# Kernel tuning notes

Measured on AMD Instinct MI355X. Metric: run time of the kernel, lower is better.

## Reference

```python
import jax, jax.numpy as jnp
import numpy as np

HEADS = 16
DIM_HEAD = 128
DIM = HEADS * DIM_HEAD          # hidden_size = 2048
SEGMENT_LEN = 496
NUM_LONGTERM = 16
NUM_PERSIST = 16
C = SEGMENT_LEN + NUM_LONGTERM  # total_segment_len = 512 (window width)
EPS = 1e-6
THETA = 10000.0
NEG = -jnp.finfo(jnp.float32).max


def _rope(t, cos, sin):
    # t: [b, h, n, d]; cos/sin: [n, d]; interleaved (rotate-half on adjacent pairs)
    t2 = t.reshape(t.shape[:-1] + (DIM_HEAD // 2, 2))
    rot = jnp.stack((-t2[..., 1], t2[..., 0]), axis=-1).reshape(t.shape)
    return t * cos + rot * sin


def _attn_bias():
    # queries: [m_len longterm-mem tokens | segment tokens]
    # keys:    [p_len persistent | m_len longterm-mem | segment tokens]
    q_len = C
    k_len = C + NUM_PERSIST
    pq = NUM_LONGTERM
    pk = NUM_PERSIST + NUM_LONGTERM
    bias = jnp.full((q_len, k_len), NEG, dtype=jnp.float32)
    bias = bias.at[:, :pk].set(0.0)  # everyone attends to the prefix
    sq = q_len - pq
    causal = jnp.tril(jnp.ones((sq, sq), dtype=bool))
    bias = bias.at[pq:, pk:].set(jnp.where(causal, 0.0, NEG))
    return bias


def setup_inputs() -> dict:
    key = jax.random.key(0)
    k1, k2, k3, k4 = jax.random.split(key, 4)
    b, n = 2, 4096  # n must be a multiple of C=512
    return {
        "x": jax.random.normal(k1, (b, n, DIM), dtype=jnp.float32),
        "norm_w": jnp.ones((DIM,), dtype=jnp.float32),
        "w_qkv": jax.random.normal(k2, (3 * DIM, DIM), dtype=jnp.float32) * 0.02,
        "w_out": jax.random.normal(k3, (DIM, DIM), dtype=jnp.float32) * 0.02,
        "pm": jax.random.normal(k4, (2, HEADS, NUM_PERSIST, DIM_HEAD), dtype=jnp.float32) * 0.02,
    }


def reference(x, norm_w, w_qkv, w_out, pm):
    b, n, d = x.shape
    # RMSNorm
    xn = x * jax.lax.rsqrt(jnp.mean(x * x, axis=-1, keepdims=True) + EPS) * norm_w
    # qkv projection (Linear, no bias)
    qkv = xn @ w_qkv.T
    q, k, v = jnp.split(qkv, 3, axis=-1)

    def to_heads(t):  # [b, n, h*d] -> [b, h, n, d]
        return t.reshape(b, n, HEADS, DIM_HEAD).transpose(0, 2, 1, 3)

    q, k, v = to_heads(q), to_heads(k), to_heads(v)

    # RoPE over full sequence positions 0..n-1 (before windowing)
    inv_freq = 1.0 / (THETA ** (jnp.arange(0, DIM_HEAD, 2, dtype=jnp.float32) / DIM_HEAD))
    freqs = jnp.arange(n, dtype=jnp.float32)[:, None] * inv_freq  # [n, d/2]
    freqs = jnp.repeat(freqs, 2, axis=-1)                          # [n, d]
    cos, sin = jnp.cos(freqs), jnp.sin(freqs)
    q = _rope(q, cos, sin)
    k = _rope(k, cos, sin)

    # split into windows of width C: [b, h, n, d] -> [(b*w), h, C, d]
    w = n // C

    def to_windows(t):
        return t.reshape(b, HEADS, w, C, DIM_HEAD).transpose(0, 2, 1, 3, 4).reshape(b * w, HEADS, C, DIM_HEAD)

    q, k, v = to_windows(q), to_windows(k), to_windows(v)

    # prepend persistent memory tokens to k, v
    pmk = jnp.broadcast_to(pm[0], (b * w, HEADS, NUM_PERSIST, DIM_HEAD))
    pmv = jnp.broadcast_to(pm[1], (b * w, HEADS, NUM_PERSIST, DIM_HEAD))
    k = jnp.concatenate((pmk, k), axis=-2)  # [(b*w), h, C+P, d]
    v = jnp.concatenate((pmv, v), axis=-2)

    bias = _attn_bias()  # [C, C+P]
    scale = DIM_HEAD ** -0.5
    sim = jnp.einsum('whqd,whkd->whqk', q, k) * scale + bias
    attn = jax.nn.softmax(sim, axis=-1)
    out = jnp.einsum('whqk,whkd->whqd', attn, v)

    # '(b w) h c d -> b (w c) (h d)'
    out = out.reshape(b, w, HEADS, C, DIM_HEAD).transpose(0, 1, 3, 2, 4).reshape(b, n, HEADS * DIM_HEAD)
    return out @ w_out.T
```

## Files before the change

### kernel.cpp

```cpp
#include <hip/hip_runtime.h>
#include <hip/hip_bf16.h>

typedef __attribute__((ext_vector_type(8))) short short8v;
typedef __attribute__((ext_vector_type(4))) float f32x4;
typedef __attribute__((ext_vector_type(4))) unsigned short us4;

#define DEV static __device__ __forceinline__

DEV unsigned short f2bf(float f) {
  unsigned u = __builtin_bit_cast(unsigned, f);
  u += 0x7FFFu + ((u >> 16) & 1u);
  return (unsigned short)(u >> 16);
}
DEV float bf2f(unsigned short s) {
  unsigned u = ((unsigned)s) << 16;
  return __builtin_bit_cast(float, u);
}
DEV void gload16(const void* g, void* l) {
  __builtin_amdgcn_global_load_lds((const __attribute__((address_space(1))) void*)g,
                                   (__attribute__((address_space(3))) void*)l, 16, 0, 0);
}

__global__ __launch_bounds__(256) void k_cvt(const float* __restrict__ s,
                                             unsigned short* __restrict__ d, long n4) {
  long i = (long)blockIdx.x * 256 + threadIdx.x;
  if (i >= n4) return;
  f32x4 v = *((const f32x4*)s + i);
  us4 o;
  o[0] = f2bf(v[0]); o[1] = f2bf(v[1]); o[2] = f2bf(v[2]); o[3] = f2bf(v[3]);
  *((us4*)d + i) = o;
}

__global__ __launch_bounds__(256) void k_pmprep(const float* __restrict__ pm,
                                                unsigned short* __restrict__ pmk,
                                                unsigned short* __restrict__ vt,
                                                unsigned short* __restrict__ zbuf) {
  int idx = blockIdx.x * 256 + threadIdx.x;
  if (idx < 8) zbuf[idx] = 0;
  if (idx >= 16 * 16 * 128) return;
  int d = idx & 127, p = (idx >> 7) & 15, h = idx >> 11;
  float kvl = pm[((0 * 16 + h) * 16 + p) * 128 + d];
  float vvl = pm[((1 * 16 + h) * 16 + p) * 128 + d];
  pmk[(h * 16 + p) * 128 + d] = f2bf(kvl);
  unsigned short vb = f2bf(vvl);
  for (int w = 0; w < 16; ++w) {
    long base = ((long)(w * 16 + h) * 128 + d) * 576;
    vt[base + p] = vb;
    vt[base + 528 + p] = 0;
    vt[base + 544 + p] = 0;
    vt[base + 560 + p] = 0;
  }
}

__global__ __launch_bounds__(256) void k_ropetab(float* __restrict__ ct, float* __restrict__ st) {
  int idx = blockIdx.x * 256 + threadIdx.x;
  int pos = idx >> 6, i = idx & 63;
  float invf = __powf(10000.f, -(float)i * (1.f / 64.f));
  float a = (float)pos * invf;
  ct[idx] = cosf(a);
  st[idx] = sinf(a);
}

__global__ __launch_bounds__(256) void k_rms(const float* __restrict__ x,
                                             const float* __restrict__ w,
                                             unsigned short* __restrict__ xb) {
  int row = blockIdx.x, tid = threadIdx.x;
  const f32x4* xr = (const f32x4*)(x + (long)row * 2048);
  f32x4 v0 = xr[tid * 2], v1 = xr[tid * 2 + 1];
  float ss = v0[0]*v0[0] + v0[1]*v0[1] + v0[2]*v0[2] + v0[3]*v0[3]
           + v1[0]*v1[0] + v1[1]*v1[1] + v1[2]*v1[2] + v1[3]*v1[3];
  ss += __shfl_xor(ss, 1);  ss += __shfl_xor(ss, 2);  ss += __shfl_xor(ss, 4);
  ss += __shfl_xor(ss, 8);  ss += __shfl_xor(ss, 16); ss += __shfl_xor(ss, 32);
  __shared__ float red[4];
  if ((tid & 63) == 0) red[tid >> 6] = ss;
  __syncthreads();
  float tot = red[0] + red[1] + red[2] + red[3];
  float rs = rsqrtf(tot * (1.f / 2048.f) + 1e-6f);
  float xv[8] = {v0[0], v0[1], v0[2], v0[3], v1[0], v1[1], v1[2], v1[3]};
  short8v pack;
#pragma unroll
  for (int j = 0; j < 8; ++j) pack[j] = (short)f2bf(xv[j] * rs * w[tid * 8 + j]);
  *((short8v*)(xb + (long)row * 2048) + tid) = pack;
}


#define VMCNT4 asm volatile("s_waitcnt vmcnt(4)" ::: "memory")
#define VMCNT0 asm volatile("s_waitcnt vmcnt(0)" ::: "memory")
#define SCHEDB __builtin_amdgcn_sched_barrier(0)
#define NOSTG ((void)0)

template <int OUTF32>
__global__ __launch_bounds__(512, 2) void k_gemm8(const unsigned short* __restrict__ A,
                                                  const unsigned short* __restrict__ B,
                                                  unsigned short* __restrict__ Cb,
                                                  float* __restrict__ Cf,
                                                  int M, int N, int K) {
  __shared__ __align__(16) unsigned short lds[4 * 256 * 64];
  const int tid = threadIdx.x;
  const int lane = tid & 63;
  const int ql = lane & 15, g = lane >> 4;
  const int wid = tid >> 6;
  const int wm = wid >> 2, wn = wid & 3;

  const int nbx = N >> 8;
  const int nwg = gridDim.x;
  int bid = blockIdx.x;
  int swz = (bid & 7) * (nwg >> 3) + (bid >> 3);
  int by = swz / nbx, bx = swz - by * nbx;
  const long rowA0 = (long)by << 8;
  const long rowB0 = (long)bx << 8;

  const int idx0 = tid, idx1 = 512 + tid;
  const int dr0 = idx0 >> 3, sc0 = (idx0 & 7) ^ (dr0 & 7);
  const int dr1 = idx1 >> 3, sc1 = (idx1 & 7) ^ (dr1 & 7);
  const long halfA = 128L * K;
  const unsigned short* pA0 = A + (rowA0 + dr0) * (long)K + sc0 * 8;
  const unsigned short* pA1 = A + (rowA0 + dr1) * (long)K + sc1 * 8;
  const unsigned short* pB0 = B + (rowB0 + dr0) * (long)K + sc0 * 8;
  const unsigned short* pB1 = B + (rowB0 + dr1) * (long)K + sc1 * 8;

  const int rsw0 = (g ^ (ql & 7)) * 8;
  const int rsw1 = ((4 + g) ^ (ql & 7)) * 8;

  short8v fa[4], fb[2][4];
  f32x4 acc[8][4] = {};

#define STAGE_A(b, h, kk) do { \
  gload16(pA0 + (long)(h) * halfA + (kk), lds + (b) * 32768 + (h) * 8192 + (idx0 << 3)); \
  gload16(pA1 + (long)(h) * halfA + (kk), lds + (b) * 32768 + (h) * 8192 + (idx1 << 3)); } while (0)
#define STAGE_B(b, h, kk) do { \
  gload16(pB0 + (long)(h) * halfA + (kk), lds + (b) * 32768 + 16384 + (h) * 8192 + (idx0 << 3)); \
  gload16(pB1 + (long)(h) * halfA + (kk), lds + (b) * 32768 + 16384 + (h) * 8192 + (idx1 << 3)); } while (0)

#define PHASE(buf, mh, ks, LOADB, STG, VMC) do { \
  { const unsigned short* p_ = lds + (buf) * 32768 + (((wm << 7) + (mh) * 64 + ql) << 6) + ((ks) ? rsw1 : rsw0); \
    _Pragma("unroll") for (int mi_ = 0; mi_ < 4; ++mi_) fa[mi_] = *(const short8v*)(p_ + (mi_ << 10)); } \
  if (LOADB) { const unsigned short* p_ = lds + (buf) * 32768 + 16384 + (((wn << 6) + ql) << 6) + ((ks) ? rsw1 : rsw0); \
    _Pragma("unroll") for (int n_ = 0; n_ < 4; ++n_) fb[ks][n_] = *(const short8v*)(p_ + (n_ << 10)); } \
  STG; \
  SCHEDB; __builtin_amdgcn_s_barrier(); SCHEDB; \
  __builtin_amdgcn_s_setprio(1); \
  _Pragma("unroll") for (int mi_ = 0; mi_ < 4; ++mi_) \
    _Pragma("unroll") for (int n_ = 0; n_ < 4; ++n_) \
      acc[(mh) * 4 + mi_][n_] = __builtin_amdgcn_mfma_f32_16x16x32_bf16(fa[mi_], fb[ks][n_], acc[(mh) * 4 + mi_][n_], 0, 0, 0); \
  __builtin_amdgcn_s_setprio(0); \
  VMC; \
  SCHEDB; __builtin_amdgcn_s_barrier(); SCHEDB; \
} while (0)

  const int NT = K >> 6;
  const int NITER = NT >> 1;

  STAGE_A(0, 0, 0); STAGE_A(0, 1, 0);
  STAGE_B(0, 0, 0); STAGE_B(0, 1, 0);
  STAGE_B(1, 0, 64); STAGE_B(1, 1, 64);
  VMCNT4;
  SCHEDB; __builtin_amdgcn_s_barrier(); SCHEDB;

  for (int i = 0; i < NITER - 1; ++i) {
    const int k1 = (2 * i + 1) << 6;
    const int k2 = (2 * i + 2) << 6;
    const int k3 = (2 * i + 3) << 6;
    PHASE(0, 0, 0, 1, STAGE_A(1, 0, k1), NOSTG);
    PHASE(0, 0, 1, 1, STAGE_A(1, 1, k1), NOSTG);
    PHASE(0, 1, 0, 0, STAGE_B(0, 0, k2), NOSTG);
    PHASE(0, 1, 1, 0, STAGE_B(0, 1, k2), VMCNT4);
    PHASE(1, 0, 0, 1, STAGE_A(0, 0, k2), NOSTG);
    PHASE(1, 0, 1, 1, STAGE_A(0, 1, k2), NOSTG);
    PHASE(1, 1, 0, 0, STAGE_B(1, 0, k3), NOSTG);
    PHASE(1, 1, 1, 0, STAGE_B(1, 1, k3), VMCNT4);
  }
  {
    const int k1 = (NT - 1) << 6;
    PHASE(0, 0, 0, 1, STAGE_A(1, 0, k1), NOSTG);
    PHASE(0, 0, 1, 1, STAGE_A(1, 1, k1), NOSTG);
    PHASE(0, 1, 0, 0, NOSTG, NOSTG);
    PHASE(0, 1, 1, 0, NOSTG, VMCNT0);
    PHASE(1, 0, 0, 1, NOSTG, NOSTG);
    PHASE(1, 0, 1, 1, NOSTG, NOSTG);
    PHASE(1, 1, 0, 0, NOSTG, NOSTG);
    PHASE(1, 1, 1, 0, NOSTG, NOSTG);
  }

#pragma unroll
  for (int am = 0; am < 8; ++am)
#pragma unroll
    for (int n = 0; n < 4; ++n)
#pragma unroll
      for (int r = 0; r < 4; ++r) {
        long row = rowA0 + (wm << 7) + am * 16 + (g << 2) + r;
        long col = rowB0 + (wn << 6) + n * 16 + ql;
        if (OUTF32) Cf[row * N + col] = acc[am][n][r];
        else        Cb[row * N + col] = f2bf(acc[am][n][r]);
      }
#undef STAGE_A
#undef STAGE_B
#undef PHASE
}

__global__ __launch_bounds__(256) void k_kprep(unsigned short* __restrict__ qkv,
                                               unsigned short* __restrict__ vt,
                                               const float* __restrict__ ct,
                                               const float* __restrict__ st) {
  __shared__ unsigned short lt[64 * 136];
  const int tile = blockIdx.x, h = blockIdx.y;
  const int tid = threadIdx.x;
  const int t0 = tile * 64;
  {
    int row = t0 + (tid >> 2);
    int d0 = (tid & 3) * 32;
    int pos = row & 4095;
    unsigned short* kp = qkv + (long)row * 6144 + 2048 + h * 128 + d0;
    const float* cp = ct + pos * 64 + (d0 >> 1);
    const float* sp = st + pos * 64 + (d0 >> 1);
    f32x4 cv[4], sv[4];
#pragma unroll
    for (int j = 0; j < 4; ++j) { cv[j] = *(const f32x4*)(cp + j * 4); sv[j] = *(const f32x4*)(sp + j * 4); }
    short8v kv[4];
#pragma unroll
    for (int j = 0; j < 4; ++j) kv[j] = *(const short8v*)(kp + j * 8);
#pragma unroll
    for (int j = 0; j < 4; ++j) {
      short8v outv;
#pragma unroll
      for (int p = 0; p < 4; ++p) {
        float a = bf2f((unsigned short)kv[j][2 * p]);
        float b = bf2f((unsigned short)kv[j][2 * p + 1]);
        float c = cv[j][p], s = sv[j][p];
        outv[2 * p]     = (short)f2bf(a * c - b * s);
        outv[2 * p + 1] = (short)f2bf(b * c + a * s);
      }
      *(short8v*)(kp + j * 8) = outv;
    }
  }
  {
    int row = tid >> 2, seg = tid & 3;
    const unsigned short* src = qkv + (long)(t0 + row) * 6144 + 4096 + h * 128 + seg * 32;
#pragma unroll
    for (int j = 0; j < 4; ++j)
      *(short8v*)(lt + row * 136 + seg * 32 + j * 8) = *(const short8v*)(src + j * 8);
  }
  __syncthreads();
  int d = tid >> 1, half = tid & 1;
  int wh = t0 >> 9;
  long dst = ((long)(wh * 16 + h) * 128 + d) * 576 + (t0 & 511) + 16 + half * 32;
  unsigned short tmp[32];
#pragma unroll
  for (int kk = 0; kk < 32; ++kk) tmp[kk] = lt[(half * 32 + kk) * 136 + d];
#pragma unroll
  for (int j = 0; j < 4; ++j) {
    short8v v;
#pragma unroll
    for (int e = 0; e < 8; ++e) v[e] = (short)tmp[j * 8 + e];
    *(short8v*)(vt + dst + j * 8) = v;
  }
}

__global__ __launch_bounds__(512) void k_attn(const unsigned short* __restrict__ qkv,
                                              const unsigned short* __restrict__ vt,
                                              const unsigned short* __restrict__ pmk,
                                              const unsigned short* __restrict__ zbuf,
                                              const float* __restrict__ ct,
                                              const float* __restrict__ stt,
                                              unsigned short* __restrict__ attno) {
  __shared__ __align__(16) unsigned short Ks[2][32 * 128];
  __shared__ __align__(16) unsigned short Vs[2][128 * 32];
  const int wh = blockIdx.x, h = blockIdx.y, qb = blockIdx.z;
  const int tid = threadIdx.x;
  const int wave = tid >> 6, lane = tid & 63;
  const int ql = lane & 15, g = lane >> 4;
  const int tokbase = (wh >> 3) * 4096 + (wh & 7) * 512;
  const int qi = qb * 128 + wave * 16 + ql;
  const int wqmin = qb * 128 + wave * 16;
  const int wqmax = wqmin + 15;
  const long qrow = (long)(tokbase + qi) * 6144;
  const int pos = (tokbase + qi) & 4095;
  short8v qf[4];
#pragma unroll
  for (int ks = 0; ks < 4; ++ks) {
    short8v qv = *(const short8v*)(qkv + qrow + h * 128 + ks * 32 + g * 8);
    f32x4 cv = *(const f32x4*)(ct + pos * 64 + ks * 16 + g * 4);
    f32x4 sv = *(const f32x4*)(stt + pos * 64 + ks * 16 + g * 4);
    const float SC = 0.08838834764831845f;
#pragma unroll
    for (int p = 0; p < 4; ++p) {
      float a = bf2f((unsigned short)qv[2 * p]);
      float b = bf2f((unsigned short)qv[2 * p + 1]);
      qf[ks][2 * p]     = (short)f2bf((a * cv[p] - b * sv[p]) * SC);
      qf[ks][2 * p + 1] = (short)f2bf((b * cv[p] + a * sv[p]) * SC);
    }
  }
  const int nkt = min(17, (qb * 128 + 144 + 31) >> 5);
  const long vbase = (long)(wh * 16 + h) * 128 * 576;

  float mrun = -3.0e38f, lrun = 0.f;
  f32x4 o[8] = {};

#define STAGEKV(kt, b) do { \
    { int kl_ = tid >> 4, dc_ = tid & 15, dcs_ = dc_ ^ (kl_ & 7); \
      int ki_ = (kt) * 32 + kl_; \
      const unsigned short* src_; \
      if (ki_ < 16)       src_ = pmk + (h * 16 + ki_) * 128 + dcs_ * 8; \
      else if (ki_ < 528) src_ = qkv + (long)(tokbase + ki_ - 16) * 6144 + 2048 + h * 128 + dcs_ * 8; \
      else                src_ = zbuf; \
      gload16(src_, &Ks[b][0] + (size_t)tid * 8); } \
    { int d_ = tid >> 2, kc_ = tid & 3, kcs_ = kc_ ^ (d_ & 3); \
      gload16(vt + vbase + (long)d_ * 576 + (kt) * 32 + kcs_ * 8, &Vs[b][0] + (size_t)tid * 8); } \
  } while (0)

  STAGEKV(0, 0);
  __syncthreads();
  for (int kt = 0; kt < nkt; ++kt) {
    const int cur = kt & 1;
    if (kt + 1 < nkt) STAGEKV(kt + 1, cur ^ 1);
    if (kt * 32 <= wqmax + 16) {
      f32x4 stv[2] = {};
      __builtin_amdgcn_s_setprio(1);
#pragma unroll
      for (int kf = 0; kf < 2; ++kf) {
        int row = kf * 16 + ql;
#pragma unroll
        for (int ks = 0; ks < 4; ++ks) {
          int chunk = (ks * 4 + g) ^ (row & 7);
          short8v kv = *(const short8v*)(&Ks[cur][0] + row * 128 + chunk * 8);
          stv[kf] = __builtin_amdgcn_mfma_f32_16x16x32_bf16(kv, qf[ks], stv[kf], 0, 0, 0);
        }
      }
      __builtin_amdgcn_s_setprio(0);
      float tmax = -3.0e38f;
      const bool needmask = !(kt == 0 || (kt * 32 + 15 <= wqmin));
      if (needmask) {
#pragma unroll
        for (int kf = 0; kf < 2; ++kf)
#pragma unroll
          for (int r = 0; r < 4; ++r) {
            int ki = kt * 32 + kf * 16 + g * 4 + r;
            bool ok = (ki < 32) || (qi >= 16 && ki <= qi + 16);
            float s = ok ? stv[kf][r] : -3.0e38f;
            stv[kf][r] = s;
            tmax = fmaxf(tmax, s);
          }
      } else {
#pragma unroll
        for (int kf = 0; kf < 2; ++kf)
#pragma unroll
          for (int r = 0; r < 4; ++r) tmax = fmaxf(tmax, stv[kf][r]);
      }
      tmax = fmaxf(tmax, __shfl_xor(tmax, 16));
      tmax = fmaxf(tmax, __shfl_xor(tmax, 32));
      if (!__all(tmax <= mrun + 8.f)) {
        float mnew = fmaxf(mrun, tmax);
        float corr = __expf(mrun - mnew);
        lrun *= corr;
#pragma unroll
        for (int db = 0; db < 8; ++db) {
          o[db][0] *= corr; o[db][1] *= corr; o[db][2] *= corr; o[db][3] *= corr;
        }
        mrun = mnew;
      }
      float psum = 0.f;
#pragma unroll
      for (int kf = 0; kf < 2; ++kf)
#pragma unroll
        for (int r = 0; r < 4; ++r) {
          float p = __expf(stv[kf][r] - mrun);
          stv[kf][r] = p;
          psum += p;
        }
      psum += __shfl_xor(psum, 16);
      psum += __shfl_xor(psum, 32);
      lrun += psum;
      short8v pb;
#pragma unroll
      for (int j = 0; j < 8; ++j) {
        int srcl = (((g & 1) * 2 + (j >> 2)) << 4) | ql;
        float v0 = __shfl(stv[0][j & 3], srcl);
        float v1 = __shfl(stv[1][j & 3], srcl);
        pb[j] = (short)f2bf((g >> 1) ? v1 : v0);
      }
      __builtin_amdgcn_s_setprio(1);
#pragma unroll
      for (int db = 0; db < 8; ++db) {
        int d = db * 16 + ql;
        int kc = g ^ (d & 3);
        short8v vf = *(const short8v*)(&Vs[cur][0] + d * 32 + kc * 8);
        o[db] = __builtin_amdgcn_mfma_f32_16x16x32_bf16(vf, pb, o[db], 0, 0, 0);
      }
      __builtin_amdgcn_s_setprio(0);
    }
    __syncthreads();
  }
#undef STAGEKV
  float inv = 1.0f / lrun;
  long obase = (long)(tokbase + qi) * 2048 + h * 128;
#pragma unroll
  for (int db = 0; db < 8; ++db)
#pragma unroll
    for (int r = 0; r < 4; ++r)
      attno[obase + db * 16 + g * 4 + r] = f2bf(o[db][r] * inv);
}

extern "C" void kernel_launch(void* const* d_in, const int* in_sizes, int n_in,
                              void* d_out, int out_size, void* d_ws, size_t ws_size,
                              hipStream_t stream) {
  const float* x      = (const float*)d_in[0];
  const float* norm_w = (const float*)d_in[1];
  const float* w_qkv  = (const float*)d_in[2];
  const float* w_out  = (const float*)d_in[3];
  const float* pm     = (const float*)d_in[4];
  float* out = (float*)d_out;

  char* ws = (char*)d_ws;
  size_t off = 0;
  auto alloc = [&](size_t bytes) -> void* {
    void* p = ws + off;
    off += (bytes + 255) & ~(size_t)255;
    return p;
  };
  unsigned short* xb    = (unsigned short*)alloc(8192ull * 2048 * 2);
  unsigned short* wqkvb = (unsigned short*)alloc(6144ull * 2048 * 2);
  unsigned short* woutb = (unsigned short*)alloc(2048ull * 2048 * 2);
  unsigned short* qkv   = (unsigned short*)alloc(8192ull * 6144 * 2);
  unsigned short* vt    = (unsigned short*)alloc(256ull * 128 * 576 * 2);
  unsigned short* attno = (unsigned short*)alloc(8192ull * 2048 * 2);
  unsigned short* pmk   = (unsigned short*)alloc(16 * 16 * 128 * 2);
  float* ct             = (float*)alloc(4096 * 64 * 4);
  float* stt            = (float*)alloc(4096 * 64 * 4);
  unsigned short* zbuf  = (unsigned short*)alloc(256);

  hipLaunchKernelGGL(k_cvt, dim3(12288), dim3(256), 0, stream, w_qkv, wqkvb, 3145728L);
  hipLaunchKernelGGL(k_cvt, dim3(4096), dim3(256), 0, stream, w_out, woutb, 1048576L);
  hipLaunchKernelGGL(k_pmprep, dim3(128), dim3(256), 0, stream, pm, pmk, vt, zbuf);
  hipLaunchKernelGGL(k_ropetab, dim3(1024), dim3(256), 0, stream, ct, stt);
  hipLaunchKernelGGL(k_rms, dim3(8192), dim3(256), 0, stream, x, norm_w, xb);
  hipLaunchKernelGGL((k_gemm8<0>), dim3(24 * 32), dim3(512), 0, stream,
                     xb, wqkvb, qkv, (float*)nullptr, 8192, 6144, 2048);
  hipLaunchKernelGGL(k_kprep, dim3(128, 16), dim3(256), 0, stream, qkv, vt, ct, stt);
  hipLaunchKernelGGL(k_attn, dim3(16, 16, 4), dim3(512), 0, stream,
                     qkv, vt, pmk, zbuf, ct, stt, attno);
  hipLaunchKernelGGL((k_gemm8<1>), dim3(8 * 32), dim3(512), 0, stream,
                     attno, woutb, (unsigned short*)nullptr, out, 8192, 2048, 2048);
}
```

Baseline: 405.9 us.

## Merge prep kernels into one launch, use LDS for P transpose, vectorize output stores

```diff
diff --git a/kernel.cpp b/kernel.cpp
--- a/kernel.cpp
+++ b/kernel.cpp
@@ -4,6 +4,7 @@
 typedef __attribute__((ext_vector_type(8))) short short8v;
 typedef __attribute__((ext_vector_type(4))) float f32x4;
 typedef __attribute__((ext_vector_type(4))) unsigned short us4;
+typedef __attribute__((ext_vector_type(4))) unsigned u32x4;
 
 #define DEV static __device__ __forceinline__
 
@@ -21,66 +22,73 @@
                                    (__attribute__((address_space(3))) void*)l, 16, 0, 0);
 }
 
-__global__ __launch_bounds__(256) void k_cvt(const float* __restrict__ s,
-                                             unsigned short* __restrict__ d, long n4) {
-  long i = (long)blockIdx.x * 256 + threadIdx.x;
-  if (i >= n4) return;
-  f32x4 v = *((const f32x4*)s + i);
-  us4 o;
-  o[0] = f2bf(v[0]); o[1] = f2bf(v[1]); o[2] = f2bf(v[2]); o[3] = f2bf(v[3]);
-  *((us4*)d + i) = o;
-}
-
-__global__ __launch_bounds__(256) void k_pmprep(const float* __restrict__ pm,
-                                                unsigned short* __restrict__ pmk,
-                                                unsigned short* __restrict__ vt,
-                                                unsigned short* __restrict__ zbuf) {
-  int idx = blockIdx.x * 256 + threadIdx.x;
-  if (idx < 8) zbuf[idx] = 0;
-  if (idx >= 16 * 16 * 128) return;
-  int d = idx & 127, p = (idx >> 7) & 15, h = idx >> 11;
-  float kvl = pm[((0 * 16 + h) * 16 + p) * 128 + d];
-  float vvl = pm[((1 * 16 + h) * 16 + p) * 128 + d];
-  pmk[(h * 16 + p) * 128 + d] = f2bf(kvl);
-  unsigned short vb = f2bf(vvl);
-  for (int w = 0; w < 16; ++w) {
-    long base = ((long)(w * 16 + h) * 128 + d) * 576;
-    vt[base + p] = vb;
-    vt[base + 528 + p] = 0;
-    vt[base + 544 + p] = 0;
-    vt[base + 560 + p] = 0;
-  }
-}
-
-__global__ __launch_bounds__(256) void k_ropetab(float* __restrict__ ct, float* __restrict__ st) {
-  int idx = blockIdx.x * 256 + threadIdx.x;
-  int pos = idx >> 6, i = idx & 63;
-  float invf = __powf(10000.f, -(float)i * (1.f / 64.f));
-  float a = (float)pos * invf;
-  ct[idx] = cosf(a);
-  st[idx] = sinf(a);
-}
-
-__global__ __launch_bounds__(256) void k_rms(const float* __restrict__ x,
-                                             const float* __restrict__ w,
-                                             unsigned short* __restrict__ xb) {
-  int row = blockIdx.x, tid = threadIdx.x;
-  const f32x4* xr = (const f32x4*)(x + (long)row * 2048);
-  f32x4 v0 = xr[tid * 2], v1 = xr[tid * 2 + 1];
-  float ss = v0[0]*v0[0] + v0[1]*v0[1] + v0[2]*v0[2] + v0[3]*v0[3]
-           + v1[0]*v1[0] + v1[1]*v1[1] + v1[2]*v1[2] + v1[3]*v1[3];
-  ss += __shfl_xor(ss, 1);  ss += __shfl_xor(ss, 2);  ss += __shfl_xor(ss, 4);
-  ss += __shfl_xor(ss, 8);  ss += __shfl_xor(ss, 16); ss += __shfl_xor(ss, 32);
+__global__ __launch_bounds__(256) void k_prep(const float* __restrict__ w_qkv,
+                                              unsigned short* __restrict__ wqkvb,
+                                              const float* __restrict__ w_out,
+                                              unsigned short* __restrict__ woutb,
+                                              const float* __restrict__ pm,
+                                              unsigned short* __restrict__ pmk,
+                                              unsigned short* __restrict__ vt,
+                                              unsigned short* __restrict__ zbuf,
+                                              float* __restrict__ ct,
+                                              float* __restrict__ st,
+                                              const float* __restrict__ x,
+                                              const float* __restrict__ norm_w,
+                                              unsigned short* __restrict__ xb) {
   __shared__ float red[4];
-  if ((tid & 63) == 0) red[tid >> 6] = ss;
-  __syncthreads();
-  float tot = red[0] + red[1] + red[2] + red[3];
-  float rs = rsqrtf(tot * (1.f / 2048.f) + 1e-6f);
-  float xv[8] = {v0[0], v0[1], v0[2], v0[3], v1[0], v1[1], v1[2], v1[3]};
-  short8v pack;
-#pragma unroll
-  for (int j = 0; j < 8; ++j) pack[j] = (short)f2bf(xv[j] * rs * w[tid * 8 + j]);
-  *((short8v*)(xb + (long)row * 2048) + tid) = pack;
+  const int b = blockIdx.x, tid = threadIdx.x;
+  if (b < 12288) {
+    long i = (long)b * 256 + tid;
+    f32x4 v = *((const f32x4*)w_qkv + i);
+    us4 o;
+    o[0] = f2bf(v[0]); o[1] = f2bf(v[1]); o[2] = f2bf(v[2]); o[3] = f2bf(v[3]);
+    *((us4*)wqkvb + i) = o;
+  } else if (b < 16384) {
+    long i = (long)(b - 12288) * 256 + tid;
+    f32x4 v = *((const f32x4*)w_out + i);
+    us4 o;
+    o[0] = f2bf(v[0]); o[1] = f2bf(v[1]); o[2] = f2bf(v[2]); o[3] = f2bf(v[3]);
+    *((us4*)woutb + i) = o;
+  } else if (b < 16512) {
+    int idx = (b - 16384) * 256 + tid;
+    if (idx < 8) zbuf[idx] = 0;
+    int d = idx & 127, p = (idx >> 7) & 15, h = idx >> 11;
+    float kvl = pm[((0 * 16 + h) * 16 + p) * 128 + d];
+    float vvl = pm[((1 * 16 + h) * 16 + p) * 128 + d];
+    pmk[(h * 16 + p) * 128 + d] = f2bf(kvl);
+    unsigned short vb = f2bf(vvl);
+    for (int w = 0; w < 16; ++w) {
+      long base = ((long)(w * 16 + h) * 128 + d) * 576;
+      vt[base + p] = vb;
+      vt[base + 528 + p] = 0;
+      vt[base + 544 + p] = 0;
+      vt[base + 560 + p] = 0;
+    }
+  } else if (b < 17536) {
+    int idx = (b - 16512) * 256 + tid;
+    int pos = idx >> 6, i = idx & 63;
+    float invf = __powf(10000.f, -(float)i * (1.f / 64.f));
+    float a = (float)pos * invf;
+    ct[idx] = cosf(a);
+    st[idx] = sinf(a);
+  } else {
+    int row = b - 17536;
+    const f32x4* xr = (const f32x4*)(x + (long)row * 2048);
+    f32x4 v0 = xr[tid * 2], v1 = xr[tid * 2 + 1];
+    float ss = v0[0]*v0[0] + v0[1]*v0[1] + v0[2]*v0[2] + v0[3]*v0[3]
+             + v1[0]*v1[0] + v1[1]*v1[1] + v1[2]*v1[2] + v1[3]*v1[3];
+    ss += __shfl_xor(ss, 1);  ss += __shfl_xor(ss, 2);  ss += __shfl_xor(ss, 4);
+    ss += __shfl_xor(ss, 8);  ss += __shfl_xor(ss, 16); ss += __shfl_xor(ss, 32);
+    if ((tid & 63) == 0) red[tid >> 6] = ss;
+    __syncthreads();
+    float tot = red[0] + red[1] + red[2] + red[3];
+    float rs = rsqrtf(tot * (1.f / 2048.f) + 1e-6f);
+    float xv[8] = {v0[0], v0[1], v0[2], v0[3], v1[0], v1[1], v1[2], v1[3]};
+    short8v pack;
+#pragma unroll
+    for (int j = 0; j < 8; ++j) pack[j] = (short)f2bf(xv[j] * rs * norm_w[tid * 8 + j]);
+    *((short8v*)(xb + (long)row * 2048) + tid) = pack;
+  }
 }
 
 
@@ -265,6 +273,7 @@
                                               unsigned short* __restrict__ attno) {
   __shared__ __align__(16) unsigned short Ks[2][32 * 128];
   __shared__ __align__(16) unsigned short Vs[2][128 * 32];
+  __shared__ unsigned Ps[8][16][16];
   const int wh = blockIdx.x, h = blockIdx.y, qb = blockIdx.z;
   const int tid = threadIdx.x;
   const int wave = tid >> 6, lane = tid & 63;
@@ -370,14 +379,21 @@
       psum += __shfl_xor(psum, 16);
       psum += __shfl_xor(psum, 32);
       lrun += psum;
-      short8v pb;
-#pragma unroll
-      for (int j = 0; j < 8; ++j) {
-        int srcl = (((g & 1) * 2 + (j >> 2)) << 4) | ql;
-        float v0 = __shfl(stv[0][j & 3], srcl);
-        float v1 = __shfl(stv[1][j & 3], srcl);
-        pb[j] = (short)f2bf((g >> 1) ? v1 : v0);
-      }
+#pragma unroll
+      for (int kf = 0; kf < 2; ++kf) {
+        unsigned w01 = (unsigned)f2bf(stv[kf][0]) | ((unsigned)f2bf(stv[kf][1]) << 16);
+        unsigned w23 = (unsigned)f2bf(stv[kf][2]) | ((unsigned)f2bf(stv[kf][3]) << 16);
+        int pr = kf * 8 + 2 * g;
+        Ps[wave][pr][ql ^ (pr & 7)] = w01;
+        Ps[wave][pr + 1][ql ^ ((pr + 1) & 7)] = w23;
+      }
+      u32x4 pbw;
+#pragma unroll
+      for (int t = 0; t < 4; ++t) {
+        int pr = 4 * g + t;
+        pbw[t] = Ps[wave][pr][ql ^ (pr & 7)];
+      }
+      short8v pb = __builtin_bit_cast(short8v, pbw);
       __builtin_amdgcn_s_setprio(1);
 #pragma unroll
       for (int db = 0; db < 8; ++db) {
@@ -394,10 +410,12 @@
   float inv = 1.0f / lrun;
   long obase = (long)(tokbase + qi) * 2048 + h * 128;
 #pragma unroll
-  for (int db = 0; db < 8; ++db)
-#pragma unroll
-    for (int r = 0; r < 4; ++r)
-      attno[obase + db * 16 + g * 4 + r] = f2bf(o[db][r] * inv);
+  for (int db = 0; db < 8; ++db) {
+    us4 ov;
+#pragma unroll
+    for (int r = 0; r < 4; ++r) ov[r] = f2bf(o[db][r] * inv);
+    *(us4*)(attno + obase + db * 16 + g * 4) = ov;
+  }
 }
 
 extern "C" void kernel_launch(void* const* d_in, const int* in_sizes, int n_in,
@@ -428,11 +446,8 @@
   float* stt            = (float*)alloc(4096 * 64 * 4);
   unsigned short* zbuf  = (unsigned short*)alloc(256);
 
-  hipLaunchKernelGGL(k_cvt, dim3(12288), dim3(256), 0, stream, w_qkv, wqkvb, 3145728L);
-  hipLaunchKernelGGL(k_cvt, dim3(4096), dim3(256), 0, stream, w_out, woutb, 1048576L);
-  hipLaunchKernelGGL(k_pmprep, dim3(128), dim3(256), 0, stream, pm, pmk, vt, zbuf);
-  hipLaunchKernelGGL(k_ropetab, dim3(1024), dim3(256), 0, stream, ct, stt);
-  hipLaunchKernelGGL(k_rms, dim3(8192), dim3(256), 0, stream, x, norm_w, xb);
+  hipLaunchKernelGGL(k_prep, dim3(25728), dim3(256), 0, stream,
+                     w_qkv, wqkvb, w_out, woutb, pm, pmk, vt, zbuf, ct, stt, x, norm_w, xb);
   hipLaunchKernelGGL((k_gemm8<0>), dim3(24 * 32), dim3(512), 0, stream,
                      xb, wqkvb, qkv, (float*)nullptr, 8192, 6144, 2048);
   hipLaunchKernelGGL(k_kprep, dim3(128, 16), dim3(256), 0, stream, qkv, vt, ct, stt);
```

Result: no change. 403.0 us (-0.7%).
